# Kernel tuning notes

Measured on AMD Instinct MI355X. Metric: run time of the kernel, lower is better.

The kernel has to match this reference:

```python
import jax, jax.numpy as jnp
import numpy as np

B, N, D = 8, 2048, 256
K = 3  # conv kernel size

def causal_conv(x, w, b):
    # x: [B, N, D] -> conv over seq with left replicate padding (causal)
    xc = jnp.transpose(x, (0, 2, 1))                       # [B, D, N]
    xc = jnp.pad(xc, ((0, 0), (0, 0), (K - 1, 0)), mode='edge')
    y = jax.lax.conv_general_dilated(
        xc, w, window_strides=(1,), padding='VALID',
        dimension_numbers=('NCH', 'OIH', 'NCH'))           # [B, Dout, N]
    y = y + b[None, :, None]
    return jnp.transpose(y, (0, 2, 1))                     # [B, N, Dout]

def setup_inputs() -> dict:
    key = jax.random.key(0)
    ks = jax.random.split(key, 5)
    query = jax.random.normal(ks[0], (B, N, D), dtype=jnp.float32)
    keys = jax.random.normal(ks[1], (B, N, D), dtype=jnp.float32)
    vals = jax.random.normal(ks[2], (B, N, D), dtype=jnp.float32)
    # causal mask [B, N, N]: attend to positions j <= i
    mask = jnp.broadcast_to(jnp.tril(jnp.ones((N, N), dtype=jnp.int32)), (B, N, N))
    conv_w = jax.random.normal(ks[3], (D, D, K), dtype=jnp.float32) * (1.0 / np.sqrt(D * K))
    conv_b = jnp.zeros((D,), dtype=jnp.float32)
    return {"query": query, "keys": keys, "vals": vals, "mask": mask,
            "conv_w": conv_w, "conv_b": conv_b}

def reference(query, keys, vals, mask, conv_w, conv_b):
    q = causal_conv(query, conv_w, conv_b)                 # [B, N, D]
    k = causal_conv(keys, conv_w, conv_b)                  # [B, N, D]
    # Euclidean pairwise distances: ||q_i - k_j||
    q2 = jnp.sum(q * q, axis=-1)                           # [B, N]
    k2 = jnp.sum(k * k, axis=-1)                           # [B, N]
    qk = jnp.einsum('bid,bjd->bij', q, k)                  # [B, N, N]
    d2 = jnp.maximum(q2[:, :, None] + k2[:, None, :] - 2.0 * qk, 0.0)
    distances = jnp.sqrt(d2)
    presoftmax = jnp.where(mask == 0, -jnp.inf, -distances)
    attn = jax.nn.softmax(presoftmax, axis=-1)             # [B, N, N]
    shifted_vals = jnp.roll(vals, shift=1, axis=1).at[:, 0, :].set(0.0)
    return jnp.einsum('bij,bjd->bid', attn, shifted_vals)  # [B, N, D]
```

## Files before the change

### kernel.cpp

```cpp
#include <hip/hip_runtime.h>

typedef _Float16 f16;
typedef _Float16 f16x4 __attribute__((ext_vector_type(4)));
typedef _Float16 f16x8 __attribute__((ext_vector_type(8)));
typedef float f32x4 __attribute__((ext_vector_type(4)));

#define NB 8
#define NS 2048
#define ND 256
#define NM (NB * NS)
#define LOG2E 1.44269504f


__device__ __forceinline__ int swzK(int row, int col) {
  return (((row) << 9) | ((col) << 1)) ^ (((row) & 7) << 4);
}

__global__ __launch_bounds__(256) void prep_kernel(
    const float* __restrict__ vals, const float* __restrict__ conv_w,
    f16* __restrict__ vT, f16* __restrict__ WkF) {
  int tid = threadIdx.x;
  if (blockIdx.x < 512) {
    __shared__ f16 Vl[32 * 256];
    int tile = blockIdx.x;
    for (int s = tid; s < 1024; s += 256) {
      int j = s >> 5, d0 = (s & 31) * 8;
      int g = tile * 32 + j;
      f16x8 h;
      if ((g & (NS - 1)) == 0) {
        for (int e = 0; e < 8; e++) h[e] = (f16)0.f;
      } else {
        const float* src = vals + (size_t)(g - 1) * ND + d0;
        f32x4 v0 = *(const f32x4*)src, v1 = *(const f32x4*)(src + 4);
        for (int e = 0; e < 4; e++) { h[e] = (f16)v0[e]; h[4 + e] = (f16)v1[e]; }
      }
      *(f16x8*)((char*)Vl + j * 512 + d0 * 2) = h;
    }
    __syncthreads();
    char* dst = (char*)vT + (size_t)tile * 16384;
    #pragma unroll
    for (int k = 0; k < 4; k++) {
      int ch = tid + k * 256;
      int lane = ch & 63;
      int d = ((ch >> 6) << 4) + (lane & 15);
      int g4c = lane >> 4;
      f16x8 h;
      #pragma unroll
      for (int js = 0; js < 2; js++)
        #pragma unroll
        for (int r = 0; r < 4; r++)
          h[js * 4 + r] = *(const f16*)((const char*)Vl + (js * 16 + 4 * g4c + r) * 512 + d * 2);
      *(f16x8*)(dst + ch * 16) = h;
    }
  } else {
    int t = (blockIdx.x - 512) * 256 + tid;
    if (t < 24576) {
      int o = t / 96, kb = t - o * 96;
      int k0 = kb * 8;
      int ks = k0 >> 5, g4w = (k0 >> 3) & 3;
      f16x8 h;
      #pragma unroll
      for (int e = 0; e < 8; e++) {
        int k = k0 + e;
        int tap = k >> 8, d = k & 255;
        h[e] = (f16)conv_w[o * 768 + d * 3 + tap];
      }
      *(f16x8*)((char*)WkF + (size_t)((((o >> 4) * 24 + ks) * 64 + (o & 15) + 16 * g4w)) * 16) = h;
    }
  }
}

__global__ __launch_bounds__(256) void conv_kernel(
    const float* __restrict__ query, const float* __restrict__ keys,
    const float* __restrict__ bias, const f16* __restrict__ WkF,
    f16* __restrict__ qT, f16* __restrict__ kT,
    float* __restrict__ q2, float* __restrict__ k2) {
  __shared__ f16 Xl[66 * 256];
  __shared__ float red[4][64];
  int bid = blockIdx.x;
  int tens = bid >> 8;
  int tile = bid & 255;
  const float* X = tens ? keys : query;
  float* Y2 = tens ? k2 : q2;
  int base = tile * 64;
  int bstart = base & ~(NS - 1);
  int tid = threadIdx.x;
  for (int c = tid; c < 66 * 32; c += 256) {
    int row = c >> 5, d0 = (c & 31) * 8;
    int g = base - 2 + row; if (g < bstart) g = bstart;
    const float* src = X + (size_t)g * ND + d0;
    f32x4 v0 = *(const f32x4*)src, v1 = *(const f32x4*)(src + 4);
    f16x8 h;
    for (int e = 0; e < 4; e++) { h[e] = (f16)v0[e]; h[4 + e] = (f16)v1[e]; }
    *(f16x8*)((char*)Xl + swzK(row, d0)) = h;
  }
  __syncthreads();
  int lane = tid & 63, w = tid >> 6;
  int c16 = lane & 15, g4 = lane >> 4;
  f32x4 acc[4][4] = {};
  const char* wb = (const char*)WkF + ((size_t)(w * 4) * 24) * 1024 + lane * 16;
  f16x8 bcur[4], bnext[4];
  #pragma unroll
  for (int nt = 0; nt < 4; nt++) bcur[nt] = *(const f16x8*)(wb + nt * 24 * 1024);
  for (int ks = 0; ks < 24; ks++) {
    if (ks < 23) {
      #pragma unroll
      for (int nt = 0; nt < 4; nt++)
        bnext[nt] = *(const f16x8*)(wb + (nt * 24 + ks + 1) * 1024);
    }
    int kk0 = ks * 32;
    int tap = kk0 >> 8, d0 = kk0 & 255;
    f16x8 afr[4];
    #pragma unroll
    for (int ms = 0; ms < 4; ms++)
      afr[ms] = *(const f16x8*)((const char*)Xl + swzK(ms * 16 + c16 + tap, d0 + 8 * g4));
    __builtin_amdgcn_s_setprio(1);
    #pragma unroll
    for (int ms = 0; ms < 4; ms++)
      #pragma unroll
      for (int nt = 0; nt < 4; nt++)
        acc[ms][nt] = __builtin_amdgcn_mfma_f32_16x16x32_f16(afr[ms], bcur[nt], acc[ms][nt], 0, 0, 0);
    __builtin_amdgcn_s_setprio(0);
    #pragma unroll
    for (int nt = 0; nt < 4; nt++) bcur[nt] = bnext[nt];
  }
  float bv[4];
  #pragma unroll
  for (int nt = 0; nt < 4; nt++) bv[nt] = bias[w * 64 + nt * 16 + c16];
  float rp[4][4];
  #pragma unroll
  for (int ms = 0; ms < 4; ms++)
    #pragma unroll
    for (int r = 0; r < 4; r++) {
      float s = 0.f;
      #pragma unroll
      for (int nt = 0; nt < 4; nt++) {
        float v = acc[ms][nt][r] + bv[nt];
        acc[ms][nt][r] = v;
        s += v * v;
      }
      rp[ms][r] = s;
    }
  #pragma unroll
  for (int off = 1; off < 16; off <<= 1)
    #pragma unroll
    for (int ms = 0; ms < 4; ms++)
      #pragma unroll
      for (int r = 0; r < 4; r++)
        rp[ms][r] += __shfl_xor(rp[ms][r], off, 64);
  if (c16 == 0)
    #pragma unroll
    for (int ms = 0; ms < 4; ms++)
      #pragma unroll
      for (int r = 0; r < 4; r++)
        red[w][ms * 16 + 4 * g4 + r] = rp[ms][r];
  __syncthreads();
  #pragma unroll
  for (int ms = 0; ms < 4; ms++)
    #pragma unroll
    for (int nt = 0; nt < 4; nt++)
      #pragma unroll
      for (int r = 0; r < 4; r++) {
        int row64 = ms * 16 + 4 * g4 + r;
        int col = w * 64 + nt * 16 + c16;
        int b;
        if (tens == 0)
          b = (row64 >> 4) * 8192 + (col >> 5) * 1024 + (row64 & 15) * 16
            + ((col >> 3) & 3) * 256 + (col & 7) * 2;
        else
          b = ((row64 >> 5) << 14) + (col >> 5) * 2048 + (((row64 >> 4) & 1) << 10)
            + (row64 & 15) * 16 + ((col >> 3) & 3) * 256 + (col & 7) * 2;
        b ^= ((b >> 7) & 7) << 4;
        *(f16*)((char*)Xl + b) = (f16)acc[ms][nt][r];
      }
  __syncthreads();
  char* dst = tens ? (char*)kT + ((size_t)(base >> 5) << 14)
                   : (char*)qT + ((size_t)(base >> 6) << 15);
  #pragma unroll
  for (int i = 0; i < 8; i++) {
    int b = tid * 128 + i * 16;
    f16x8 v = *(const f16x8*)((const char*)Xl + (b ^ (((b >> 7) & 7) << 4)));
    *(f16x8*)(dst + b) = v;
  }
  if (tid < 64)
    Y2[base + tid] = red[0][tid] + red[1][tid] + red[2][tid] + red[3][tid];
}

__global__ __launch_bounds__(64) void attn_kernel(
    const f16* __restrict__ qT, const f16* __restrict__ kT,
    const f16* __restrict__ vT, const float* __restrict__ q2,
    const float* __restrict__ k2, float* __restrict__ out,
    f16* __restrict__ partO, float2* __restrict__ partML, int TT, int S1) {
  int nwg = gridDim.x;
  int orig = blockIdx.x;
  int lg = (orig & 7) * (nwg >> 3) + (orig >> 3);
  int wq = lg & 3;
  int gc = lg >> 2;
  int ci = gc % S1, b = gc / S1;
  int itile = 0, pref = 0;
  for (int i = 0; i < 32; i++) {
    int cnt = (2 * (i + 1) + TT - 1) / TT;
    if (ci < pref + cnt) { itile = i; break; }
    pref += cnt;
  }
  int jc = ci - pref;
  int nc = (2 * (itile + 1) + TT - 1) / TT;
  int t0 = jc * TT;
  int t1 = min(t0 + TT, 2 * (itile + 1));
  int lane = threadIdx.x & 63;
  int c16 = lane & 15, g4 = lane >> 4;
  int rowbase = b * NS + itile * 64;
  int qrow = rowbase + wq * 16 + c16;
  int iglob = itile * 64 + wq * 16 + c16;
  f16x8 qf[8];
  {
    const char* qb = (const char*)qT + ((size_t)(b * 32 + itile) << 15)
                   + (wq << 13) + lane * 16;
    #pragma unroll
    for (int ks = 0; ks < 8; ks++)
      qf[ks] = *(const f16x8*)(qb + ks * 1024);
  }
  float q2v = q2[qrow];
  f32x4 o4[16] = {};
  float m_run = -1e30f, l_run = 0.f;
  const char* tb = (const char*)kT + ((size_t)(b * 64 + t0) << 14) + lane * 16;
  const char* vb = (const char*)vT + ((size_t)(b * 64 + t0) << 14) + lane * 16;
  for (int jt = t0; jt < t1; jt++) {
    int jb = b * NS + jt * 32;
    int jbs = jt * 32;
    f32x4 s4[2] = {};
    #pragma unroll
    for (int h = 0; h < 2; h++) {
      f16x8 kf[4][2];
      #pragma unroll
      for (int ks = 0; ks < 4; ks++) {
        kf[ks][0] = *(const f16x8*)(tb + (h * 4 + ks) * 2048);
        kf[ks][1] = *(const f16x8*)(tb + (h * 4 + ks) * 2048 + 1024);
      }
      __builtin_amdgcn_s_setprio(1);
      #pragma unroll
      for (int ks = 0; ks < 4; ks++) {
        s4[0] = __builtin_amdgcn_mfma_f32_16x16x32_f16(kf[ks][0], qf[h * 4 + ks], s4[0], 0, 0, 0);
        s4[1] = __builtin_amdgcn_mfma_f32_16x16x32_f16(kf[ks][1], qf[h * 4 + ks], s4[1], 0, 0, 0);
      }
      __builtin_amdgcn_s_setprio(0);
    }
    f16x8 vv[8];
    #pragma unroll
    for (int nt = 0; nt < 8; nt++)
      vv[nt] = *(const f16x8*)(vb + nt * 1024);
    tb += 16384;
    float p[2][4];
    float mt = -1e30f;
    #pragma unroll
    for (int js = 0; js < 2; js++) {
      f32x4 k2v = *(const f32x4*)(k2 + jb + js * 16 + 4 * g4);
      #pragma unroll
      for (int r = 0; r < 4; r++) {
        int jsq = jbs + js * 16 + 4 * g4 + r;
        float d2 = fmaxf(q2v + k2v[r] - 2.f * s4[js][r], 0.f);
        float lg_ = -sqrtf(d2);
        if (jsq > iglob) lg_ = -1e30f;
        p[js][r] = lg_;
        mt = fmaxf(mt, lg_);
      }
    }
    mt = fmaxf(mt, __shfl_xor(mt, 16, 64));
    mt = fmaxf(mt, __shfl_xor(mt, 32, 64));
    if (!__all(mt <= m_run + 4.f)) {
      float m_new = fmaxf(m_run, mt);
      float scale = exp2f((m_run - m_new) * LOG2E);
      l_run *= scale;
      m_run = m_new;
      f32x4 sc;
      #pragma unroll
      for (int r = 0; r < 4; r++) sc[r] = __shfl(scale, 4 * g4 + r, 64);
      #pragma unroll
      for (int nt = 0; nt < 16; nt++)
        #pragma unroll
        for (int r = 0; r < 4; r++) o4[nt][r] *= sc[r];
    }
    f16x4 pa[2];
    #pragma unroll
    for (int js = 0; js < 2; js++)
      #pragma unroll
      for (int r = 0; r < 4; r++) {
        float pv = exp2f((p[js][r] - m_run) * LOG2E);
        l_run += pv;
        pa[js][r] = (f16)pv;
      }
    __builtin_amdgcn_s_setprio(1);
    #pragma unroll
    for (int nt = 0; nt < 8; nt++) {
      f16x4 vb0, vb1;
      #pragma unroll
      for (int r = 0; r < 4; r++) { vb0[r] = vv[nt][r]; vb1[r] = vv[nt][4 + r]; }
      o4[nt] = __builtin_amdgcn_mfma_f32_16x16x16f16(pa[0], vb0, o4[nt], 0, 0, 0);
      o4[nt] = __builtin_amdgcn_mfma_f32_16x16x16f16(pa[1], vb1, o4[nt], 0, 0, 0);
    }
    __builtin_amdgcn_s_setprio(0);
    #pragma unroll
    for (int nt = 0; nt < 8; nt++)
      vv[nt] = *(const f16x8*)(vb + (8 + nt) * 1024);
    vb += 16384;
    __builtin_amdgcn_s_setprio(1);
    #pragma unroll
    for (int nt = 0; nt < 8; nt++) {
      f16x4 vb0, vb1;
      #pragma unroll
      for (int r = 0; r < 4; r++) { vb0[r] = vv[nt][r]; vb1[r] = vv[nt][4 + r]; }
      o4[8 + nt] = __builtin_amdgcn_mfma_f32_16x16x16f16(pa[0], vb0, o4[8 + nt], 0, 0, 0);
      o4[8 + nt] = __builtin_amdgcn_mfma_f32_16x16x16f16(pa[1], vb1, o4[8 + nt], 0, 0, 0);
    }
    __builtin_amdgcn_s_setprio(0);
  }
  l_run += __shfl_xor(l_run, 16, 64);
  l_run += __shfl_xor(l_run, 32, 64);
  float inv = 1.f / l_run;
  f32x4 li;
  #pragma unroll
  for (int r = 0; r < 4; r++) li[r] = __shfl(inv, 4 * g4 + r, 64);
  if (nc == 1) {
    #pragma unroll
    for (int nt = 0; nt < 16; nt++)
      #pragma unroll
      for (int r = 0; r < 4; r++) {
        int irow = rowbase + wq * 16 + 4 * g4 + r;
        out[(size_t)irow * ND + nt * 16 + c16] = o4[nt][r] * li[r];
      }
  } else {
    if (g4 == 0)
      partML[(size_t)gc * 64 + wq * 16 + c16] = make_float2(m_run, l_run);
    char* pb = (char*)partO + ((size_t)gc << 15);
    #pragma unroll
    for (int q = 0; q < 8; q++) {
      f16x8 h;
      #pragma unroll
      for (int e = 0; e < 8; e++) {
        int nt = 2 * q + (e >> 2), r = e & 3;
        h[e] = (f16)(o4[nt][r] * li[r]);
      }
      *(f16x8*)(pb + q * 4096 + (wq * 64 + lane) * 16) = h;
    }
  }
}

__global__ __launch_bounds__(256) void combine_kernel(
    const f16* __restrict__ partO, const float2* __restrict__ partML,
    float* __restrict__ out, int TT, int S1) {
  int per = 32 - TT / 2;
  int cq = blockIdx.x & 3;
  int rest = blockIdx.x >> 2;
  int b = rest / per;
  int itile = TT / 2 + rest % per;
  int nc = (2 * (itile + 1) + TT - 1) / TT;
  int pref = 0;
  for (int i = 0; i < itile; i++) pref += (2 * (i + 1) + TT - 1) / TT;
  size_t pbase = (size_t)b * S1 + pref;
  int tid = threadIdx.x, lane = tid & 63, w = tid >> 6;
  int c16 = lane & 15, g4 = lane >> 4;
  int mlrow = w * 16 + 4 * g4;
  float M[4] = {-1e30f, -1e30f, -1e30f, -1e30f};
  for (int c = 0; c < nc; ++c)
    #pragma unroll
    for (int r = 0; r < 4; r++)
      M[r] = fmaxf(M[r], partML[(pbase + c) * 64 + mlrow + r].x);
  float acc[16];
  #pragma unroll
  for (int i = 0; i < 16; i++) acc[i] = 0.f;
  float L[4] = {0.f, 0.f, 0.f, 0.f};
  for (int c = 0; c < nc; ++c) {
    float wcr[4];
    #pragma unroll
    for (int r = 0; r < 4; r++) {
      float2 ml = partML[(pbase + c) * 64 + mlrow + r];
      wcr[r] = ml.y * exp2f((ml.x - M[r]) * LOG2E);
      L[r] += wcr[r];
    }
    const char* pb = (const char*)partO + ((pbase + c) << 15);
    #pragma unroll
    for (int qh = 0; qh < 2; qh++) {
      int q = 2 * cq + qh;
      f16x8 v = *(const f16x8*)(pb + q * 4096 + tid * 16);
      #pragma unroll
      for (int e = 0; e < 8; e++) {
        int ntl = 2 * qh + (e >> 2), r = e & 3;
        acc[ntl * 4 + r] += wcr[r] * (float)v[e];
      }
    }
  }
  #pragma unroll
  for (int r = 0; r < 4; r++) L[r] = 1.f / L[r];
  #pragma unroll
  for (int ntl = 0; ntl < 4; ntl++)
    #pragma unroll
    for (int r = 0; r < 4; r++) {
      int irow = b * NS + itile * 64 + mlrow + r;
      out[(size_t)irow * ND + (4 * cq + ntl) * 16 + c16] = acc[ntl * 4 + r] * L[r];
    }
}

extern "C" void kernel_launch(void* const* d_in, const int* in_sizes, int n_in,
                              void* d_out, int out_size, void* d_ws, size_t ws_size,
                              hipStream_t stream) {
  const float* query  = (const float*)d_in[0];
  const float* keys   = (const float*)d_in[1];
  const float* vals   = (const float*)d_in[2];
  const float* conv_w = (const float*)d_in[4];
  const float* conv_b = (const float*)d_in[5];
  char* ws = (char*)d_ws;
  f16*   qT  = (f16*)(ws);
  f16*   kT  = (f16*)(ws + (size_t)8 * 1024 * 1024);
  f16*   vT  = (f16*)(ws + (size_t)16 * 1024 * 1024);
  f16*   WkF = (f16*)(ws + (size_t)24 * 1024 * 1024);
  float* q2  = (float*)(ws + (size_t)24 * 1024 * 1024 + 512 * 1024);
  float* k2  = (float*)(ws + (size_t)24 * 1024 * 1024 + 576 * 1024);
  f16*   partO = (f16*)(ws + (size_t)25 * 1024 * 1024);
  float* out = (float*)d_out;

  const int TT = 8;
  int S1 = 0;
  for (int i = 0; i < 32; i++) S1 += (2 * (i + 1) + TT - 1) / TT;
  float2* partML = (float2*)(ws + (size_t)25 * 1024 * 1024 + (size_t)S1 * 8 * 32768);

  prep_kernel<<<608, 256, 0, stream>>>(vals, conv_w, vT, WkF);
  conv_kernel<<<512, 256, 0, stream>>>(query, keys, conv_b, WkF, qT, kT, q2, k2);
  attn_kernel<<<8 * S1 * 4, 64, 0, stream>>>(qT, kT, vT, q2, k2, out,
                                             partO, partML, TT, S1);
  combine_kernel<<<8 * (32 - TT / 2) * 4, 256, 0, stream>>>(partO, partML, out, TT, S1);
}
```

Before: 109.0 us.

## Share K/V tiles across four waves via double-buffered LDS DMA loads

The attention kernel now runs as 256-thread workgroups where four waves (one per 16-row query slice) share each K and V tile. Tiles are staged into double-buffered LDS with global_load_lds DMA, and the next tile is prefetched while the current one is computed. Previously each single-wave workgroup read the same K/V tiles from global memory on its own. The change adds a __syncthreads per tile and LDS pressure (64KB), which may reduce occupancy, and it drops the s_setprio hints.

```diff
diff --git a/kernel.cpp b/kernel.cpp
--- a/kernel.cpp
+++ b/kernel.cpp
@@ -4,6 +4,8 @@
 typedef _Float16 f16x4 __attribute__((ext_vector_type(4)));
 typedef _Float16 f16x8 __attribute__((ext_vector_type(8)));
 typedef float f32x4 __attribute__((ext_vector_type(4)));
+typedef const __attribute__((address_space(1))) unsigned int* gptr1;
+typedef __attribute__((address_space(3))) unsigned int* lptr3;
 
 #define NB 8
 #define NS 2048
@@ -14,6 +16,9 @@
 
 __device__ __forceinline__ int swzK(int row, int col) {
   return (((row) << 9) | ((col) << 1)) ^ (((row) & 7) << 4);
+}
+__device__ __forceinline__ void dma16(const void* g, void* l) {
+  __builtin_amdgcn_global_load_lds((gptr1)g, (lptr3)l, 16, 0, 0);
 }
 
 __global__ __launch_bounds__(256) void prep_kernel(
@@ -186,16 +191,16 @@
     Y2[base + tid] = red[0][tid] + red[1][tid] + red[2][tid] + red[3][tid];
 }
 
-__global__ __launch_bounds__(64) void attn_kernel(
+__global__ __launch_bounds__(256) void attn_kernel(
     const f16* __restrict__ qT, const f16* __restrict__ kT,
     const f16* __restrict__ vT, const float* __restrict__ q2,
     const float* __restrict__ k2, float* __restrict__ out,
     f16* __restrict__ partO, float2* __restrict__ partML, int TT, int S1) {
+  __shared__ f16 Kb[2][8192];
+  __shared__ f16 Vb[2][8192];
   int nwg = gridDim.x;
   int orig = blockIdx.x;
-  int lg = (orig & 7) * (nwg >> 3) + (orig >> 3);
-  int wq = lg & 3;
-  int gc = lg >> 2;
+  int gc = (orig & 7) * (nwg >> 3) + (orig >> 3);
   int ci = gc % S1, b = gc / S1;
   int itile = 0, pref = 0;
   for (int i = 0; i < 32; i++) {
@@ -207,7 +212,7 @@
   int nc = (2 * (itile + 1) + TT - 1) / TT;
   int t0 = jc * TT;
   int t1 = min(t0 + TT, 2 * (itile + 1));
-  int lane = threadIdx.x & 63;
+  int tid = threadIdx.x, lane = tid & 63, wq = tid >> 6;
   int c16 = lane & 15, g4 = lane >> 4;
   int rowbase = b * NS + itile * 64;
   int qrow = rowbase + wq * 16 + c16;
@@ -223,33 +228,52 @@
   float q2v = q2[qrow];
   f32x4 o4[16] = {};
   float m_run = -1e30f, l_run = 0.f;
-  const char* tb = (const char*)kT + ((size_t)(b * 64 + t0) << 14) + lane * 16;
-  const char* vb = (const char*)vT + ((size_t)(b * 64 + t0) << 14) + lane * 16;
+  {
+    size_t toff = (size_t)(b * 64 + t0) << 14;
+    const char* gk = (const char*)kT + toff + wq * 4096 + lane * 16;
+    const char* gv = (const char*)vT + toff + wq * 4096 + lane * 16;
+    char* lk = (char*)&Kb[0][0] + wq * 4096;
+    char* lv = (char*)&Vb[0][0] + wq * 4096;
+    #pragma unroll
+    for (int i = 0; i < 4; i++) {
+      dma16(gk + i * 1024, lk + i * 1024);
+      dma16(gv + i * 1024, lv + i * 1024);
+    }
+  }
+  __syncthreads();
+  int cur = 0;
   for (int jt = t0; jt < t1; jt++) {
+    if (jt + 1 < t1) {
+      size_t toff = (size_t)(b * 64 + jt + 1) << 14;
+      const char* gk = (const char*)kT + toff + wq * 4096 + lane * 16;
+      const char* gv = (const char*)vT + toff + wq * 4096 + lane * 16;
+      char* lk = (char*)&Kb[cur ^ 1][0] + wq * 4096;
+      char* lv = (char*)&Vb[cur ^ 1][0] + wq * 4096;
+      #pragma unroll
+      for (int i = 0; i < 4; i++) {
+        dma16(gk + i * 1024, lk + i * 1024);
+        dma16(gv + i * 1024, lv + i * 1024);
+      }
+    }
     int jb = b * NS + jt * 32;
     int jbs = jt * 32;
+    const char* kl = (const char*)&Kb[cur][0] + lane * 16;
+    const char* vl = (const char*)&Vb[cur][0] + lane * 16;
     f32x4 s4[2] = {};
     #pragma unroll
     for (int h = 0; h < 2; h++) {
       f16x8 kf[4][2];
       #pragma unroll
       for (int ks = 0; ks < 4; ks++) {
-        kf[ks][0] = *(const f16x8*)(tb + (h * 4 + ks) * 2048);
-        kf[ks][1] = *(const f16x8*)(tb + (h * 4 + ks) * 2048 + 1024);
-      }
-      __builtin_amdgcn_s_setprio(1);
+        kf[ks][0] = *(const f16x8*)(kl + (h * 4 + ks) * 2048);
+        kf[ks][1] = *(const f16x8*)(kl + (h * 4 + ks) * 2048 + 1024);
+      }
       #pragma unroll
       for (int ks = 0; ks < 4; ks++) {
         s4[0] = __builtin_amdgcn_mfma_f32_16x16x32_f16(kf[ks][0], qf[h * 4 + ks], s4[0], 0, 0, 0);
         s4[1] = __builtin_amdgcn_mfma_f32_16x16x32_f16(kf[ks][1], qf[h * 4 + ks], s4[1], 0, 0, 0);
       }
-      __builtin_amdgcn_s_setprio(0);
-    }
-    f16x8 vv[8];
-    #pragma unroll
-    for (int nt = 0; nt < 8; nt++)
-      vv[nt] = *(const f16x8*)(vb + nt * 1024);
-    tb += 16384;
+    }
     float p[2][4];
     float mt = -1e30f;
     #pragma unroll
@@ -289,7 +313,10 @@
         l_run += pv;
         pa[js][r] = (f16)pv;
       }
-    __builtin_amdgcn_s_setprio(1);
+    f16x8 vv[8];
+    #pragma unroll
+    for (int nt = 0; nt < 8; nt++)
+      vv[nt] = *(const f16x8*)(vl + nt * 1024);
     #pragma unroll
     for (int nt = 0; nt < 8; nt++) {
       f16x4 vb0, vb1;
@@ -298,12 +325,9 @@
       o4[nt] = __builtin_amdgcn_mfma_f32_16x16x16f16(pa[0], vb0, o4[nt], 0, 0, 0);
       o4[nt] = __builtin_amdgcn_mfma_f32_16x16x16f16(pa[1], vb1, o4[nt], 0, 0, 0);
     }
-    __builtin_amdgcn_s_setprio(0);
     #pragma unroll
     for (int nt = 0; nt < 8; nt++)
-      vv[nt] = *(const f16x8*)(vb + (8 + nt) * 1024);
-    vb += 16384;
-    __builtin_amdgcn_s_setprio(1);
+      vv[nt] = *(const f16x8*)(vl + (8 + nt) * 1024);
     #pragma unroll
     for (int nt = 0; nt < 8; nt++) {
       f16x4 vb0, vb1;
@@ -312,7 +336,8 @@
       o4[8 + nt] = __builtin_amdgcn_mfma_f32_16x16x16f16(pa[0], vb0, o4[8 + nt], 0, 0, 0);
       o4[8 + nt] = __builtin_amdgcn_mfma_f32_16x16x16f16(pa[1], vb1, o4[8 + nt], 0, 0, 0);
     }
-    __builtin_amdgcn_s_setprio(0);
+    __syncthreads();
+    cur ^= 1;
   }
   l_run += __shfl_xor(l_run, 16, 64);
   l_run += __shfl_xor(l_run, 32, 64);
@@ -340,7 +365,7 @@
         int nt = 2 * q + (e >> 2), r = e & 3;
         h[e] = (f16)(o4[nt][r] * li[r]);
       }
-      *(f16x8*)(pb + q * 4096 + (wq * 64 + lane) * 16) = h;
+      *(f16x8*)(pb + q * 4096 + tid * 16) = h;
     }
   }
 }
@@ -425,7 +450,7 @@
 
   prep_kernel<<<608, 256, 0, stream>>>(vals, conv_w, vT, WkF);
   conv_kernel<<<512, 256, 0, stream>>>(query, keys, conv_b, WkF, qT, kT, q2, k2);
-  attn_kernel<<<8 * S1 * 4, 64, 0, stream>>>(qT, kT, vT, q2, k2, out,
-                                             partO, partML, TT, S1);
+  attn_kernel<<<8 * S1, 256, 0, stream>>>(qT, kT, vT, q2, k2, out,
+                                          partO, partML, TT, S1);
   combine_kernel<<<8 * (32 - TT / 2) * 4, 256, 0, stream>>>(partO, partML, out, TT, S1);
 }
```

After: 107.8 us. About the same (-1.1%).
